# Optimization experiments

Measured on AMD Instinct MI355X. Metric: run time of the kernel, lower is better.

The kernel has to match this reference:

```python
import jax, jax.numpy as jnp
import numpy as np

P, S, N, D, TH = 16, 16, 128, 512, 1.0  # patch, stride, num_patch, out_dim, threshold


def setup_inputs() -> dict:
    key = jax.random.key(0)
    k1, k2 = jax.random.split(key)
    x = jax.random.normal(k1, (4, 3, 256, 256), dtype=jnp.float32)
    mask = jnp.ones((4, 1, 256, 256), dtype=jnp.float32)
    pos = jax.random.normal(k2, (4, 512, 256, 256), dtype=jnp.float32)
    return {"x": x, "mask": mask, "pos": pos}


def _gather_patches(t, idx, nw):
    # Extract only the sampled patches (fused alternative to unfold+gather).
    # t: [b, c, h, w], idx: [b, n] flat patch indices in unfold column order.
    b, c = t.shape[0], t.shape[1]
    ri = (idx // nw) * S                      # [b, n] top row of each patch
    ci = (idx % nw) * S                       # [b, n] left col of each patch
    hh = ri[:, :, None] + jnp.arange(P)       # [b, n, p]
    ww = ci[:, :, None] + jnp.arange(P)       # [b, n, p]
    bi = jnp.arange(b)[:, None, None, None, None]
    cc = jnp.arange(c)[None, None, :, None, None]
    # [b, n, c, p, p] -- channel-major flatten matches F.unfold row layout
    return t[bi, cc, hh[:, :, None, :, None], ww[:, :, None, None, :]]


def reference(x, mask, pos):
    b, c, h, w = x.shape
    nw = (w - P) // S + 1
    nh = (h - P) // S + 1
    L = nh * nw  # number of unfold columns (patches)
    # mean of each mask patch == avg pool (replaces unfold(mask).mean(dim=1))
    msum = jax.lax.reduce_window(mask[:, 0], 0.0, jax.lax.add, (1, P, P), (1, S, S), 'VALID')
    valid = (msum.reshape(b, L) / (P * P)) >= TH  # [b, L] bool
    # multinomial without replacement over 0/1 weights == Gumbel top-k over valid set
    g = jax.random.gumbel(jax.random.key(42), (b, L), dtype=jnp.float32)
    scores = jnp.where(valid, g, -jnp.inf)
    idx = jnp.sort(jax.lax.top_k(scores, N)[1], axis=-1)  # [b, N], sorted as in torch.sort
    # gather only the N sampled patches directly from x (no full im2col buffer)
    x_sample = _gather_patches(x, idx, nw).reshape(b, N, c * P * P)  # [b, N, c*p*p]
    # torch.gather with idx_pos [b, D, N] reads only the first D rows of pos_unfold,
    # i.e. the first ceil(D/p^2) channels of pos.
    kch = -(-D // (P * P))
    pos_sample = _gather_patches(pos[:, :kch], idx, nw).reshape(b, N, kch * P * P)[:, :, :D]
    return x_sample, pos_sample
```

## Files before the change

kernel.cpp:

```cpp
#include <hip/hip_runtime.h>

#define RNG_VARIANT 0

constexpr int PP = 16;
constexpr int NSEL = 128;
constexpr int B = 4, C = 3, H = 256, W = 256;
constexpr int L = 256;

__device__ __forceinline__ unsigned rotl32(unsigned x, int d) {
  return (x << d) | (x >> (32 - d));
}

__device__ __forceinline__ void threefry2x32(unsigned k0, unsigned k1,
                                             unsigned& x0, unsigned& x1) {
  unsigned ks[3] = {k0, k1, k0 ^ k1 ^ 0x1BD11BDAu};
  x0 += ks[0];
  x1 += ks[1];
  const int rot[2][4] = {{13, 15, 26, 6}, {17, 29, 16, 24}};
#pragma unroll
  for (int i = 0; i < 5; ++i) {
    const int* r = rot[i & 1];
#pragma unroll
    for (int j = 0; j < 4; ++j) {
      x0 += x1;
      x1 = rotl32(x1, r[j]);
      x1 ^= x0;
    }
    x0 += ks[(i + 1) % 3];
    x1 += ks[(i + 2) % 3] + (unsigned)(i + 1);
  }
}

__global__ void mask_sum_kernel(const float* __restrict__ mask,
                                float* __restrict__ msum) {
  int p = blockIdx.x;
  int b = p >> 8, l = p & 255;
  int ri = (l >> 4) << 4, ci = (l & 15) << 4;
  int t = threadIdx.x;
  int r = t >> 2, c4 = (t & 3) << 2;
  const float4 v = *reinterpret_cast<const float4*>(
      mask + ((size_t)b * H + ri + r) * W + ci + c4);
  float s = v.x + v.y + v.z + v.w;
#pragma unroll
  for (int off = 32; off > 0; off >>= 1) s += __shfl_down(s, off);
  if (t == 0) msum[p] = s;
}

__global__ void select_kernel(const float* __restrict__ msum,
                              int* __restrict__ idx_out) {
  int b = blockIdx.x;
  int l = threadIdx.x;
  int i = b * L + l;

  unsigned bits;
#if RNG_VARIANT == 0
  {
    unsigned x0 = 0u, x1 = (unsigned)i;
    threefry2x32(0u, 42u, x0, x1);
    bits = x0 ^ x1;
  }
#elif RNG_VARIANT == 1
  {
    int j = (i < 512) ? i : i - 512;
    unsigned x0 = (unsigned)j, x1 = (unsigned)(512 + j);
    threefry2x32(0u, 42u, x0, x1);
    bits = (i < 512) ? x0 : x1;
  }
#elif RNG_VARIANT == 2
  {
    unsigned x0 = 0u, x1 = (unsigned)i;
    threefry2x32(0u, 42u, x0, x1);
    bits = x0;
  }
#else
  {
    unsigned x0 = (unsigned)i, x1 = 0u;
    threefry2x32(0u, 42u, x0, x1);
    bits = x0 ^ x1;
  }
#endif

  bool valid = (msum[i] * (1.0f / 256.0f)) >= 1.0f;
  unsigned score = valid ? ((bits >> 9) + 1u) : 0u;

  __shared__ unsigned s_score[L];
  __shared__ unsigned char s_sel[L];
  s_score[l] = score;
  __syncthreads();

  int rank = 0;
  for (int m = 0; m < L; ++m) {
    unsigned sm = s_score[m];
    rank += (sm > score) || (sm == score && m < l);
  }
  int selected = (rank < NSEL) ? 1 : 0;
  s_sel[l] = (unsigned char)selected;
  __syncthreads();

  if (selected) {
    int slot = 0;
    for (int m = 0; m < l; ++m) slot += s_sel[m];
    idx_out[b * NSEL + slot] = l;
  }
}

__global__ void gather_kernel(const float* __restrict__ x,
                              const float* __restrict__ pos,
                              const int* __restrict__ idx,
                              float4* __restrict__ out) {
  int t = blockIdx.x * blockDim.x + threadIdx.x;
  const int XQ = B * NSEL * (C * PP * PP) / 4;
  if (t < XQ) {
    const int perb = NSEL * 192;
    int b = t / perb;
    int rem = t - b * perb;
    int n = rem / 192;
    int q = rem - n * 192;
    int d = q << 2;
    int c = d >> 8;
    int dd = d & 255;
    int pr = dd >> 4;
    int pc = dd & 15;
    int id = idx[b * NSEL + n];
    int ri = (id >> 4) << 4, ci = (id & 15) << 4;
    out[t] = *reinterpret_cast<const float4*>(
        x + (((size_t)(b * C + c)) * H + ri + pr) * W + ci + pc);
  } else {
    int u = t - XQ;
    const int perb = NSEL * 128;
    int b = u / perb;
    int rem = u - b * perb;
    int n = rem / 128;
    int q = rem - n * 128;
    int d = q << 2;
    int ch = d >> 8;
    int dd = d & 255;
    int pr = dd >> 4;
    int pc = dd & 15;
    int id = idx[b * NSEL + n];
    int ri = (id >> 4) << 4, ci = (id & 15) << 4;
    out[XQ + u] = *reinterpret_cast<const float4*>(
        pos + (((size_t)(b * 512 + ch)) * H + ri + pr) * W + ci + pc);
  }
}

extern "C" void kernel_launch(void* const* d_in, const int* in_sizes, int n_in,
                              void* d_out, int out_size, void* d_ws, size_t ws_size,
                              hipStream_t stream) {
  const float* x = (const float*)d_in[0];
  const float* mask = (const float*)d_in[1];
  const float* pos = (const float*)d_in[2];
  float* msum = (float*)d_ws;
  int* idx = (int*)((char*)d_ws + 4096);

  mask_sum_kernel<<<B * L, 64, 0, stream>>>(mask, msum);
  select_kernel<<<B, L, 0, stream>>>(msum, idx);

  const int total_f4 = (B * NSEL * (C * PP * PP) + B * NSEL * 512) / 4;
  gather_kernel<<<(total_f4 + 255) / 256, 256, 0, stream>>>(
      x, pos, idx, (float4*)d_out);
}
```

Measured before the change: 22.07 us.

## Fuse mask patch sum into select kernel and use ballot-based compaction

Removes the separate mask-sum kernel launch. Each thread of the select kernel now sums its own 16x16 mask patch with float4 loads. Rank counting reads shared memory as uint4, and output slots come from wavefront ballot/popcount plus per-wave counts instead of a serial prefix scan. The trade-off is that only 4 blocks now each read 256 KB of mask with strided per-thread loads, so that part may be slow, in exchange for one fewer launch and less serial work.

```diff
diff --git a/kernel.cpp b/kernel.cpp
--- a/kernel.cpp
+++ b/kernel.cpp
@@ -1,6 +1,4 @@
 #include <hip/hip_runtime.h>
-
-#define RNG_VARIANT 0
 
 constexpr int PP = 16;
 constexpr int NSEL = 128;
@@ -31,77 +29,54 @@
   }
 }
 
-__global__ void mask_sum_kernel(const float* __restrict__ mask,
-                                float* __restrict__ msum) {
-  int p = blockIdx.x;
-  int b = p >> 8, l = p & 255;
-  int ri = (l >> 4) << 4, ci = (l & 15) << 4;
-  int t = threadIdx.x;
-  int r = t >> 2, c4 = (t & 3) << 2;
-  const float4 v = *reinterpret_cast<const float4*>(
-      mask + ((size_t)b * H + ri + r) * W + ci + c4);
-  float s = v.x + v.y + v.z + v.w;
-#pragma unroll
-  for (int off = 32; off > 0; off >>= 1) s += __shfl_down(s, off);
-  if (t == 0) msum[p] = s;
-}
-
-__global__ void select_kernel(const float* __restrict__ msum,
+__global__ void select_kernel(const float* __restrict__ mask,
                               int* __restrict__ idx_out) {
   int b = blockIdx.x;
   int l = threadIdx.x;
-  int i = b * L + l;
+  int ri = (l >> 4) << 4, ci = (l & 15) << 4;
 
-  unsigned bits;
-#if RNG_VARIANT == 0
-  {
-    unsigned x0 = 0u, x1 = (unsigned)i;
-    threefry2x32(0u, 42u, x0, x1);
-    bits = x0 ^ x1;
+  const float* base = mask + ((size_t)b * H + ri) * W + ci;
+  float s = 0.0f;
+#pragma unroll
+  for (int r = 0; r < PP; ++r) {
+#pragma unroll
+    for (int c4 = 0; c4 < 4; ++c4) {
+      const float4 v = *reinterpret_cast<const float4*>(base + r * W + c4 * 4);
+      s += v.x + v.y + v.z + v.w;
+    }
   }
-#elif RNG_VARIANT == 1
-  {
-    int j = (i < 512) ? i : i - 512;
-    unsigned x0 = (unsigned)j, x1 = (unsigned)(512 + j);
-    threefry2x32(0u, 42u, x0, x1);
-    bits = (i < 512) ? x0 : x1;
-  }
-#elif RNG_VARIANT == 2
-  {
-    unsigned x0 = 0u, x1 = (unsigned)i;
-    threefry2x32(0u, 42u, x0, x1);
-    bits = x0;
-  }
-#else
-  {
-    unsigned x0 = (unsigned)i, x1 = 0u;
-    threefry2x32(0u, 42u, x0, x1);
-    bits = x0 ^ x1;
-  }
-#endif
+  bool valid = (s * (1.0f / 256.0f)) >= 1.0f;
 
-  bool valid = (msum[i] * (1.0f / 256.0f)) >= 1.0f;
+  unsigned x0 = 0u, x1 = (unsigned)(b * L + l);
+  threefry2x32(0u, 42u, x0, x1);
+  unsigned bits = x0 ^ x1;
   unsigned score = valid ? ((bits >> 9) + 1u) : 0u;
 
   __shared__ unsigned s_score[L];
-  __shared__ unsigned char s_sel[L];
+  __shared__ int s_wcnt[4];
   s_score[l] = score;
   __syncthreads();
 
   int rank = 0;
-  for (int m = 0; m < L; ++m) {
-    unsigned sm = s_score[m];
-    rank += (sm > score) || (sm == score && m < l);
+  const uint4* sv = reinterpret_cast<const uint4*>(s_score);
+#pragma unroll 8
+  for (int m4 = 0; m4 < L / 4; ++m4) {
+    uint4 v = sv[m4];
+    int m = m4 << 2;
+    rank += (v.x > score) || (v.x == score && (m + 0) < l);
+    rank += (v.y > score) || (v.y == score && (m + 1) < l);
+    rank += (v.z > score) || (v.z == score && (m + 2) < l);
+    rank += (v.w > score) || (v.w == score && (m + 3) < l);
   }
-  int selected = (rank < NSEL) ? 1 : 0;
-  s_sel[l] = (unsigned char)selected;
+  bool selected = rank < NSEL;
+
+  unsigned long long mball = __ballot(selected);
+  int w = l >> 6, lane = l & 63;
+  if (lane == 0) s_wcnt[w] = __popcll(mball);
   __syncthreads();
-
-  if (selected) {
-    int slot = 0;
-    for (int m = 0; m < l; ++m) slot += s_sel[m];
-    idx_out[b * NSEL + slot] = l;
-  }
+  int slot = __popcll(mball & ((1ull << lane) - 1ull));
+  for (int j = 0; j < 4; ++j) slot += (j < w) ? s_wcnt[j] : 0;
+  if (selected) idx_out[b * NSEL + slot] = l;
 }
 
 __global__ void gather_kernel(const float* __restrict__ x,
@@ -150,11 +125,9 @@
   const float* x = (const float*)d_in[0];
   const float* mask = (const float*)d_in[1];
   const float* pos = (const float*)d_in[2];
-  float* msum = (float*)d_ws;
-  int* idx = (int*)((char*)d_ws + 4096);
+  int* idx = (int*)d_ws;
 
-  mask_sum_kernel<<<B * L, 64, 0, stream>>>(mask, msum);
-  select_kernel<<<B, L, 0, stream>>>(msum, idx);
+  select_kernel<<<B, L, 0, stream>>>(mask, idx);
 
   const int total_f4 = (B * NSEL * (C * PP * PP) + B * NSEL * 512) / 4;
   gather_kernel<<<(total_f4 + 255) / 256, 256, 0, stream>>>(
```

New measurement: 19.95 us. 1.11x faster.
